# Performance work log

Hardware: AMD Instinct MI355X
Metric: run time of the kernel (lower is better)

## Reference

```python
import jax, jax.numpy as jnp
import numpy as np

NUM_HEADS = 16
WINDOW = 256  # local_window_size: query i attends keys in [i-WINDOW+1, i]


def setup_inputs() -> dict:
    key = jax.random.key(0)
    ks = jax.random.split(key, 7)
    B, L, D = 2, 2048, 1024
    s = 0.02  # typical init scale for projection weights
    return {
        "hidden_states": jax.random.normal(ks[0], (B, L, D), jnp.float32),
        "Wq": jax.random.normal(ks[1], (D, D), jnp.float32) * s,
        "bq": jnp.zeros((D,), jnp.float32),
        "Wk": jax.random.normal(ks[2], (D, D), jnp.float32) * s,
        "bk": jnp.zeros((D,), jnp.float32),
        "Wv": jax.random.normal(ks[3], (D, D), jnp.float32) * s,
        "bv": jnp.zeros((D,), jnp.float32),
    }


def reference(hidden_states, Wq, bq, Wk, bk, Wv, bv):
    B, L, D = hidden_states.shape
    H = NUM_HEADS
    dh = D // H

    def split_heads(x):  # [B,L,D] -> [B,H,L,dh]
        return x.reshape(B, L, H, dh).transpose(0, 2, 1, 3)

    q = split_heads(hidden_states @ Wq + bq)
    k = split_heads(hidden_states @ Wk + bk)
    v = split_heads(hidden_states @ Wv + bv)

    scores = jnp.einsum("bhqd,bhkd->bhqk", q, k) / jnp.sqrt(jnp.float32(dh))

    # causal sliding-window band: key j visible to query i iff i-WINDOW < j <= i
    i = jnp.arange(L)[:, None]
    j = jnp.arange(L)[None, :]
    band = (j <= i) & (j > i - WINDOW)
    scores = jnp.where(band, scores, -jnp.inf)

    probs = jax.nn.softmax(scores, axis=-1)  # dropout p=0 (eval)
    out = jnp.einsum("bhqk,bhkd->bhqd", probs, v)
    return out.transpose(0, 2, 1, 3).reshape(B, L, D)
```

## Files before the change

### kernel.cpp

```cpp
#include <hip/hip_runtime.h>
#include <hip/hip_bf16.h>
#include <stdint.h>
#include <math.h>

typedef __bf16 bf16;
typedef bf16  bf16x4  __attribute__((ext_vector_type(4)));
typedef bf16  bf16x8  __attribute__((ext_vector_type(8)));
typedef float floatx4 __attribute__((ext_vector_type(4)));

#define MFMA_16x16x32_BF16(a, b, c) \
  __builtin_amdgcn_mfma_f32_16x16x32_bf16((a), (b), (c), 0, 0, 0)

__device__ __forceinline__ int imin(int a, int b) { return a < b ? a : b; }
__device__ __forceinline__ int imax(int a, int b) { return a > b ? a : b; }

__device__ __forceinline__ void load_lds16(const void* g, void* l) {
  __builtin_amdgcn_global_load_lds(
      (const __attribute__((address_space(1))) unsigned int*)g,
      (__attribute__((address_space(3))) unsigned int*)l, 16, 0, 0);
}

#define LSEQ 2048
#define DMODEL 1024
#define NH 16
#define DH 64

__global__ void pack_all(const float4* __restrict__ x, uint16_t* __restrict__ y,
                         const float* __restrict__ Wq, const float* __restrict__ Wk,
                         const float* __restrict__ Wv, uint16_t* __restrict__ Wt) {
  const int bi = blockIdx.x;
  if (bi < 4096) {
    int i = bi * 256 + threadIdx.x;
    float4 f = x[i];
    bf16x4 v;
    v[0] = (bf16)f.x; v[1] = (bf16)f.y; v[2] = (bf16)f.z; v[3] = (bf16)f.w;
    *(bf16x4*)&y[(size_t)i * 4] = v;
    return;
  }
  __shared__ float tile[32][33];
  const int p = bi - 4096;
  const int z = p >> 10;
  const int rem = p & 1023;
  const int k0 = (rem >> 5) * 32, n0 = (rem & 31) * 32;
  const float* W = (z == 0) ? Wq : (z == 1) ? Wk : Wv;
  const int tx = threadIdx.x & 31, ty = threadIdx.x >> 5;
#pragma unroll
  for (int i = 0; i < 4; ++i)
    tile[ty + i * 8][tx] = W[(size_t)(k0 + ty + i * 8) * DMODEL + n0 + tx];
  __syncthreads();
  uint16_t* out = Wt + (size_t)z * DMODEL * DMODEL;
#pragma unroll
  for (int i = 0; i < 4; ++i)
    *(bf16*)&out[(size_t)(n0 + ty + i * 8) * DMODEL + k0 + tx] =
        (bf16)tile[tx][ty + i * 8];
}

__global__ __launch_bounds__(256, 3) void qkv_gemm(
    const uint16_t* __restrict__ A, const uint16_t* __restrict__ Wt,
    const float* __restrict__ bq, const float* __restrict__ bk,
    const float* __restrict__ bv,
    uint16_t* __restrict__ outq, uint16_t* __restrict__ outk,
    uint16_t* __restrict__ outvt) {
  __shared__ __attribute__((aligned(16))) uint16_t lds[17408];
  const int xcd = blockIdx.x & 7;
  const int i = blockIdx.x >> 3;
  const int m0 = (xcd * 4 + (i & 3)) * 128;
  const int rest = i >> 2;
  const int n0 = (rest & 7) * 128;
  const int z = rest >> 3;
  const uint16_t* Bt = Wt + (size_t)z * DMODEL * DMODEL;
  const float* bias = (z == 0) ? bq : (z == 1) ? bk : bv;

  const int t = threadIdx.x;
  const int lane = t & 63;
  const int wave = t >> 6;
  const int wm = (wave >> 1) * 64;
  const int wn = (wave & 1) * 64;
  const int col = lane & 15;
  const int quad = lane >> 4;

  floatx4 acc[4][4] = {};

  auto stage = [&](int kk, int bi) {
    const int k0 = kk * 32;
    uint16_t* base = &lds[bi * 8192];
#pragma unroll
    for (int c = 0; c < 4; ++c) {
      int chunk = t + c * 256;
      int cc = chunk & 511;
      int row = cc >> 2;
      int col16 = (cc & 3) ^ (row & 3);
      const uint16_t* g = (chunk < 512)
          ? A  + (size_t)(m0 + row) * DMODEL + k0 + col16 * 8
          : Bt + (size_t)(n0 + row) * DMODEL + k0 + col16 * 8;
      load_lds16(g, &base[chunk * 8]);
    }
  };

  stage(0, 0);
  for (int kk = 0; kk < 32; ++kk) {
    __syncthreads();
    if (kk < 31) stage(kk + 1, (kk + 1) & 1);
    const uint16_t* base = &lds[(kk & 1) * 8192];

    bf16x8 afrag[4], bfrag[4];
#pragma unroll
    for (int mi = 0; mi < 4; ++mi) {
      int r = wm + mi * 16 + col;
      afrag[mi] = *(const bf16x8*)&base[r * 32 + ((quad ^ (r & 3)) * 8)];
    }
#pragma unroll
    for (int nj = 0; nj < 4; ++nj) {
      int r = wn + nj * 16 + col;
      bfrag[nj] = *(const bf16x8*)&base[4096 + r * 32 + ((quad ^ (r & 3)) * 8)];
    }
#pragma unroll
    for (int mi = 0; mi < 4; ++mi)
#pragma unroll
      for (int nj = 0; nj < 4; ++nj)
        acc[mi][nj] = MFMA_16x16x32_BF16(afrag[mi], bfrag[nj], acc[mi][nj]);
  }

  if (z != 2) {
    const float scale = (z == 0) ? 0.125f : 1.0f;
    uint16_t* outp = (z == 0) ? outq : outk;
#pragma unroll
    for (int nj = 0; nj < 4; ++nj) {
      int gn = n0 + wn + nj * 16 + col;
      float bb = bias[gn];
      int h = gn >> 6, d = gn & 63;
#pragma unroll
      for (int mi = 0; mi < 4; ++mi) {
#pragma unroll
        for (int r = 0; r < 4; ++r) {
          int gm = m0 + wm + mi * 16 + quad * 4 + r;
          int b = gm >> 11, l = gm & 2047;
          *(bf16*)&outp[(((size_t)b * NH + h) * LSEQ + l) * DH + d] =
              (bf16)((acc[mi][nj][r] + bb) * scale);
        }
      }
    }
  } else {
    __syncthreads();
#pragma unroll
    for (int nj = 0; nj < 4; ++nj) {
      int n = wn + nj * 16 + col;
      float bb = bias[n0 + n];
#pragma unroll
      for (int mi = 0; mi < 4; ++mi) {
        int mb = wm + mi * 16 + quad * 4;
        int pp = (mb & ~31) | (((mb >> 2) & 3) << 3) | (((mb >> 4) & 1) << 2);
#pragma unroll
        for (int r = 0; r < 4; ++r)
          *(bf16*)&lds[n * 136 + pp + r] = (bf16)(acc[mi][nj][r] + bb);
      }
    }
    __syncthreads();
    const int n = t >> 1, mh = (t & 1) * 64;
    const int gn = n0 + n, d = gn & 63, h = gn >> 6;
    const int b = m0 >> 11, l0 = (m0 & 2047) + mh;
    uint16_t* dst = &outvt[(((size_t)b * NH + h) * DH + d) * LSEQ + l0];
    const uint16_t* src = &lds[n * 136 + mh];
#pragma unroll
    for (int j = 0; j < 8; ++j)
      *(bf16x8*)&dst[j * 8] = *(const bf16x8*)&src[j * 8];
  }
}

__global__ __launch_bounds__(256, 4) void attn(
    const uint16_t* __restrict__ Q, const uint16_t* __restrict__ K,
    const uint16_t* __restrict__ Vt, float* __restrict__ out) {
  __shared__ __attribute__((aligned(16))) uint16_t kbuf[2][4096];
  __shared__ __attribute__((aligned(16))) uint16_t vbuf[2][4096];

  const int t = threadIdx.x;
  const int lane = t & 63;
  const int w = t >> 6;
  const int xcd = blockIdx.x & 7;
  const int slot = blockIdx.x >> 3;
  const int bh = xcd * 4 + (slot >> 5);
  const int q0 = (slot & 31) * 64;
  const int q0w = q0 + w * 16;
  const int b = bh >> 4, h = bh & 15;
  const uint16_t* Qp = Q + (size_t)bh * LSEQ * DH;
  const uint16_t* Kp = K + (size_t)bh * LSEQ * DH;
  const uint16_t* Vp = Vt + (size_t)bh * DH * LSEQ;
  const int col = lane & 15, quad = lane >> 4;

  bf16x8 qf0 = *(const bf16x8*)&Qp[(size_t)(q0w + col) * DH + quad * 8];
  bf16x8 qf1 = *(const bf16x8*)&Qp[(size_t)(q0w + col) * DH + 32 + quad * 8];

  bf16x8 ones;
#pragma unroll
  for (int u = 0; u < 8; ++u) ones[u] = (bf16)1.0f;

  const int c_start = (q0 < 256) ? ((256 - q0) >> 6) : 0;

  floatx4 o[4] = {};
  floatx4 lac = {0.f, 0.f, 0.f, 0.f};

  auto stage = [&](int c, int bi) {
    const int kc = q0 - 256 + 64 * c;
    int ci = w * 64 + lane;
    {
      int row = ci >> 3, s = ci & 7;
      const uint16_t* g = Kp + (size_t)(kc + row) * DH + ((s ^ (row & 7)) * 8);
      load_lds16(g, &kbuf[bi][w * 512]);
      int row2 = row + 32;
      const uint16_t* g2 = Kp + (size_t)(kc + row2) * DH + ((s ^ (row2 & 7)) * 8);
      load_lds16(g2, &kbuf[bi][2048 + w * 512]);
    }
    {
      int d = ci >> 3, s = ci & 7;
      const uint16_t* g = Vp + (size_t)d * LSEQ + kc + ((s ^ (d & 7)) * 8);
      load_lds16(g, &vbuf[bi][w * 512]);
      int d2 = d + 32;
      const uint16_t* g2 = Vp + (size_t)d2 * LSEQ + kc + ((s ^ (d2 & 7)) * 8);
      load_lds16(g2, &vbuf[bi][2048 + w * 512]);
    }
  };

  stage(c_start, c_start & 1);

  for (int c = c_start; c <= 4; ++c) {
    __syncthreads();
    if (c < 4) stage(c + 1, (c + 1) & 1);

    const int kc = q0 - 256 + 64 * c;
    const int hi = q0w + 15, lo = q0w - 255;
    if (kc <= hi && kc + 64 > lo) {
      const uint16_t* kb_ = kbuf[c & 1];
      const uint16_t* vb_ = vbuf[c & 1];

      floatx4 sT[4] = {{0,0,0,0},{0,0,0,0},{0,0,0,0},{0,0,0,0}};
#pragma unroll
      for (int sub = 0; sub < 4; ++sub) {
        int r_ = sub * 16 + col;
        bf16x8 ka  = *(const bf16x8*)&kb_[r_ * 64 + ((quad ^ (r_ & 7)) * 8)];
        bf16x8 kb2 = *(const bf16x8*)&kb_[r_ * 64 + (((4 + quad) ^ (r_ & 7)) * 8)];
        sT[sub] = MFMA_16x16x32_BF16(ka, qf0, sT[sub]);
        sT[sub] = MFMA_16x16x32_BF16(kb2, qf1, sT[sub]);
      }

      const bool needm = (kc < q0w - 240) | (kc + 63 > q0w);
      const int q = q0w + col;
      bf16x8 pb[2];
#pragma unroll
      for (int sel = 0; sel < 2; ++sel) {
#pragma unroll
        for (int sp = 0; sp < 2; ++sp) {
#pragma unroll
          for (int r = 0; r < 4; ++r) {
            float v = sT[sel * 2 + sp][r];
            if (needm) {
              int key = kc + sel * 32 + sp * 16 + quad * 4 + r;
              v = ((key <= q) & (key > q - 256)) ? v : -INFINITY;
            }
            pb[sel][sp * 4 + r] = (bf16)__expf(v);
          }
        }
      }

#pragma unroll
      for (int nj = 0; nj < 4; ++nj) {
        int d = nj * 16 + col;
        bf16x8 va0 = *(const bf16x8*)&vb_[d * 64 + ((quad ^ (d & 7)) * 8)];
        bf16x8 va1 = *(const bf16x8*)&vb_[d * 64 + (((4 + quad) ^ (d & 7)) * 8)];
        o[nj] = MFMA_16x16x32_BF16(va0, pb[0], o[nj]);
        o[nj] = MFMA_16x16x32_BF16(va1, pb[1], o[nj]);
      }
      lac = MFMA_16x16x32_BF16(ones, pb[0], lac);
      lac = MFMA_16x16x32_BF16(ones, pb[1], lac);
    }
  }

  float rinv = 1.0f / lac[0];
#pragma unroll
  for (int nj = 0; nj < 4; ++nj) {
    float4 v4;
    v4.x = o[nj][0] * rinv; v4.y = o[nj][1] * rinv;
    v4.z = o[nj][2] * rinv; v4.w = o[nj][3] * rinv;
    *(float4*)&out[((size_t)b * LSEQ + q0w + col) * DMODEL + h * DH + nj * 16 + quad * 4] = v4;
  }
}

extern "C" void kernel_launch(void* const* d_in, const int* in_sizes, int n_in,
                              void* d_out, int out_size, void* d_ws, size_t ws_size,
                              hipStream_t stream) {
  const float* hidden = (const float*)d_in[0];
  const float* Wq = (const float*)d_in[1];
  const float* bq = (const float*)d_in[2];
  const float* Wk = (const float*)d_in[3];
  const float* bk = (const float*)d_in[4];
  const float* Wv = (const float*)d_in[5];
  const float* bv = (const float*)d_in[6];
  float* out = (float*)d_out;

  char* ws = (char*)d_ws;
  uint16_t* hb  = (uint16_t*)(ws);
  uint16_t* Wt  = (uint16_t*)(ws + ((size_t)8  << 20));
  uint16_t* qb  = (uint16_t*)(ws + ((size_t)14 << 20));
  uint16_t* kb  = (uint16_t*)(ws + ((size_t)22 << 20));
  uint16_t* vtb = (uint16_t*)(ws + ((size_t)30 << 20));

  pack_all<<<7168, 256, 0, stream>>>((const float4*)hidden, hb, Wq, Wk, Wv, Wt);
  qkv_gemm<<<768, 256, 0, stream>>>(hb, Wt, bq, bk, bv, qb, kb, vtb);
  attn<<<1024, 256, 0, stream>>>(qb, kb, vtb, out);
}
```

Before: 133.7 us.

## Fuse fp32-to-bf16 conversion of activations into QKV GEMM; add MFMA setprio

The separate pass that converts the hidden states to bf16 is removed. The QKV GEMM now streams fp32 activation tiles into LDS with a new XOR swizzle and converts them to bf16 when building the MFMA fragments. This drops one kernel's full write and re-read of the activation tensor, but each GEMM block loads twice the A bytes and uses more LDS, which may lower occupancy. The attention kernel also raises wave priority around its MFMA sections so matrix work is scheduled ahead of the softmax exp code.

```diff
diff --git a/kernel.cpp b/kernel.cpp
--- a/kernel.cpp
+++ b/kernel.cpp
@@ -25,20 +25,10 @@
 #define NH 16
 #define DH 64
 
-__global__ void pack_all(const float4* __restrict__ x, uint16_t* __restrict__ y,
-                         const float* __restrict__ Wq, const float* __restrict__ Wk,
-                         const float* __restrict__ Wv, uint16_t* __restrict__ Wt) {
-  const int bi = blockIdx.x;
-  if (bi < 4096) {
-    int i = bi * 256 + threadIdx.x;
-    float4 f = x[i];
-    bf16x4 v;
-    v[0] = (bf16)f.x; v[1] = (bf16)f.y; v[2] = (bf16)f.z; v[3] = (bf16)f.w;
-    *(bf16x4*)&y[(size_t)i * 4] = v;
-    return;
-  }
+__global__ void pack_w(const float* __restrict__ Wq, const float* __restrict__ Wk,
+                       const float* __restrict__ Wv, uint16_t* __restrict__ Wt) {
   __shared__ float tile[32][33];
-  const int p = bi - 4096;
+  const int p = blockIdx.x;
   const int z = p >> 10;
   const int rem = p & 1023;
   const int k0 = (rem >> 5) * 32, n0 = (rem & 31) * 32;
@@ -56,12 +46,13 @@
 }
 
 __global__ __launch_bounds__(256, 3) void qkv_gemm(
-    const uint16_t* __restrict__ A, const uint16_t* __restrict__ Wt,
+    const float* __restrict__ A,
+    const uint16_t* __restrict__ Wt,
     const float* __restrict__ bq, const float* __restrict__ bk,
     const float* __restrict__ bv,
     uint16_t* __restrict__ outq, uint16_t* __restrict__ outk,
     uint16_t* __restrict__ outvt) {
-  __shared__ __attribute__((aligned(16))) uint16_t lds[17408];
+  __shared__ __attribute__((aligned(16))) uint16_t lds[24576];
   const int xcd = blockIdx.x & 7;
   const int i = blockIdx.x >> 3;
   const int m0 = (xcd * 4 + (i & 3)) * 128;
@@ -83,17 +74,22 @@
 
   auto stage = [&](int kk, int bi) {
     const int k0 = kk * 32;
-    uint16_t* base = &lds[bi * 8192];
-#pragma unroll
-    for (int c = 0; c < 4; ++c) {
+    uint16_t* base = &lds[bi * 12288];
+#pragma unroll
+    for (int c = 0; c < 6; ++c) {
       int chunk = t + c * 256;
-      int cc = chunk & 511;
-      int row = cc >> 2;
-      int col16 = (cc & 3) ^ (row & 3);
-      const uint16_t* g = (chunk < 512)
-          ? A  + (size_t)(m0 + row) * DMODEL + k0 + col16 * 8
-          : Bt + (size_t)(n0 + row) * DMODEL + k0 + col16 * 8;
-      load_lds16(g, &base[chunk * 8]);
+      if (chunk < 1024) {
+        int row = chunk >> 3, sl = chunk & 7;
+        int cg = sl ^ (row & 7);
+        const float* g = A + (size_t)(m0 + row) * DMODEL + k0 + cg * 4;
+        load_lds16(g, &base[chunk * 8]);
+      } else {
+        int cb = chunk - 1024;
+        int row = cb >> 2, sl = cb & 3;
+        int cg = sl ^ (row & 3) ^ ((row >> 2) & 1);
+        const uint16_t* g = Bt + (size_t)(n0 + row) * DMODEL + k0 + cg * 8;
+        load_lds16(g, &base[8192 + cb * 8]);
+      }
     }
   };
 
@@ -101,18 +97,27 @@
   for (int kk = 0; kk < 32; ++kk) {
     __syncthreads();
     if (kk < 31) stage(kk + 1, (kk + 1) & 1);
-    const uint16_t* base = &lds[(kk & 1) * 8192];
+    const uint16_t* base = &lds[(kk & 1) * 12288];
 
     bf16x8 afrag[4], bfrag[4];
 #pragma unroll
     for (int mi = 0; mi < 4; ++mi) {
       int r = wm + mi * 16 + col;
-      afrag[mi] = *(const bf16x8*)&base[r * 32 + ((quad ^ (r & 3)) * 8)];
+      int f = r & 7;
+      floatx4 fa = *(const floatx4*)&base[r * 64 + (((2 * quad) ^ f) * 8)];
+      floatx4 fb = *(const floatx4*)&base[r * 64 + (((2 * quad + 1) ^ f) * 8)];
+      bf16x8 af;
+      af[0] = (bf16)fa[0]; af[1] = (bf16)fa[1];
+      af[2] = (bf16)fa[2]; af[3] = (bf16)fa[3];
+      af[4] = (bf16)fb[0]; af[5] = (bf16)fb[1];
+      af[6] = (bf16)fb[2]; af[7] = (bf16)fb[3];
+      afrag[mi] = af;
     }
 #pragma unroll
     for (int nj = 0; nj < 4; ++nj) {
       int r = wn + nj * 16 + col;
-      bfrag[nj] = *(const bf16x8*)&base[4096 + r * 32 + ((quad ^ (r & 3)) * 8)];
+      int f = (r & 3) ^ ((r >> 2) & 1);
+      bfrag[nj] = *(const bf16x8*)&base[8192 + r * 32 + ((quad ^ f) * 8)];
     }
 #pragma unroll
     for (int mi = 0; mi < 4; ++mi)
@@ -233,6 +238,7 @@
       const uint16_t* vb_ = vbuf[c & 1];
 
       floatx4 sT[4] = {{0,0,0,0},{0,0,0,0},{0,0,0,0},{0,0,0,0}};
+      __builtin_amdgcn_s_setprio(1);
 #pragma unroll
       for (int sub = 0; sub < 4; ++sub) {
         int r_ = sub * 16 + col;
@@ -241,6 +247,7 @@
         sT[sub] = MFMA_16x16x32_BF16(ka, qf0, sT[sub]);
         sT[sub] = MFMA_16x16x32_BF16(kb2, qf1, sT[sub]);
       }
+      __builtin_amdgcn_s_setprio(0);
 
       const bool needm = (kc < q0w - 240) | (kc + 63 > q0w);
       const int q = q0w + col;
@@ -261,6 +268,7 @@
         }
       }
 
+      __builtin_amdgcn_s_setprio(1);
 #pragma unroll
       for (int nj = 0; nj < 4; ++nj) {
         int d = nj * 16 + col;
@@ -271,6 +279,7 @@
       }
       lac = MFMA_16x16x32_BF16(ones, pb[0], lac);
       lac = MFMA_16x16x32_BF16(ones, pb[1], lac);
+      __builtin_amdgcn_s_setprio(0);
     }
   }
 
@@ -297,13 +306,12 @@
   float* out = (float*)d_out;
 
   char* ws = (char*)d_ws;
-  uint16_t* hb  = (uint16_t*)(ws);
-  uint16_t* Wt  = (uint16_t*)(ws + ((size_t)8  << 20));
-  uint16_t* qb  = (uint16_t*)(ws + ((size_t)14 << 20));
-  uint16_t* kb  = (uint16_t*)(ws + ((size_t)22 << 20));
-  uint16_t* vtb = (uint16_t*)(ws + ((size_t)30 << 20));
-
-  pack_all<<<7168, 256, 0, stream>>>((const float4*)hidden, hb, Wq, Wk, Wv, Wt);
-  qkv_gemm<<<768, 256, 0, stream>>>(hb, Wt, bq, bk, bv, qb, kb, vtb);
+  uint16_t* Wt  = (uint16_t*)(ws);
+  uint16_t* qb  = (uint16_t*)(ws + ((size_t)6  << 20));
+  uint16_t* kb  = (uint16_t*)(ws + ((size_t)14 << 20));
+  uint16_t* vtb = (uint16_t*)(ws + ((size_t)22 << 20));
+
+  pack_w<<<3072, 256, 0, stream>>>(Wq, Wk, Wv, Wt);
+  qkv_gemm<<<768, 256, 0, stream>>>(hidden, Wt, bq, bk, bv, qb, kb, vtb);
   attn<<<1024, 256, 0, stream>>>(qb, kb, vtb, out);
 }
```

After: 136.4 us. 1.02x slower.

## Rewrite QKV GEMM with 256x256 tiles, 8 waves, and phased ping-pong schedule

Applied to the files above, without the earlier changes.

Replaces the 128x128-tile QKV GEMM (768 blocks of 256 threads) with 256x256 tiles using 512 threads and a K-step of 64. Loads of the next A and B tiles are split across phases of the compute, with explicit waitcnt, barriers and raised wave priority around MFMA bursts. The aim is more operand reuse per LDS read and better overlap of global loads with MFMA. Only 192 blocks are launched, which may underfill the CUs. The attention kernel also gets setprio hints around its MFMA sections.

```diff
diff --git a/kernel.cpp b/kernel.cpp
--- a/kernel.cpp
+++ b/kernel.cpp
@@ -10,9 +10,6 @@
 
 #define MFMA_16x16x32_BF16(a, b, c) \
   __builtin_amdgcn_mfma_f32_16x16x32_bf16((a), (b), (c), 0, 0, 0)
-
-__device__ __forceinline__ int imin(int a, int b) { return a < b ? a : b; }
-__device__ __forceinline__ int imax(int a, int b) { return a > b ? a : b; }
 
 __device__ __forceinline__ void load_lds16(const void* g, void* l) {
   __builtin_amdgcn_global_load_lds(
@@ -55,71 +52,152 @@
         (bf16)tile[tx][ty + i * 8];
 }
 
-__global__ __launch_bounds__(256, 3) void qkv_gemm(
+__global__ __launch_bounds__(512, 2) void qkv_gemm8(
     const uint16_t* __restrict__ A, const uint16_t* __restrict__ Wt,
     const float* __restrict__ bq, const float* __restrict__ bk,
     const float* __restrict__ bv,
     uint16_t* __restrict__ outq, uint16_t* __restrict__ outk,
     uint16_t* __restrict__ outvt) {
-  __shared__ __attribute__((aligned(16))) uint16_t lds[17408];
+  __shared__ __attribute__((aligned(16))) uint16_t lds[65536];
+
   const int xcd = blockIdx.x & 7;
   const int i = blockIdx.x >> 3;
-  const int m0 = (xcd * 4 + (i & 3)) * 128;
-  const int rest = i >> 2;
-  const int n0 = (rest & 7) * 128;
-  const int z = rest >> 3;
+  const int m0 = (xcd * 2 + (i & 1)) * 256;
+  const int nz = i >> 1;
+  const int n0 = (nz & 3) * 256;
+  const int z = nz >> 2;
   const uint16_t* Bt = Wt + (size_t)z * DMODEL * DMODEL;
   const float* bias = (z == 0) ? bq : (z == 1) ? bk : bv;
 
   const int t = threadIdx.x;
   const int lane = t & 63;
-  const int wave = t >> 6;
-  const int wm = (wave >> 1) * 64;
-  const int wn = (wave & 1) * 64;
+  const int w = t >> 6;
+  const int wm = (w >> 2) * 128;
+  const int wn = (w & 3) * 64;
   const int col = lane & 15;
   const int quad = lane >> 4;
 
-  floatx4 acc[4][4] = {};
-
-  auto stage = [&](int kk, int bi) {
-    const int k0 = kk * 32;
-    uint16_t* base = &lds[bi * 8192];
+  floatx4 acc[8][4] = {};
+
+  auto stage = [&](int kt, int bi, int part) {
+    const int k0 = kt * 64;
+    uint16_t* base = &lds[bi * 32768 + part * 16384];
+    const uint16_t* src = part ? (Bt + (size_t)n0 * DMODEL)
+                               : (A  + (size_t)m0 * DMODEL);
 #pragma unroll
     for (int c = 0; c < 4; ++c) {
-      int chunk = t + c * 256;
-      int cc = chunk & 511;
-      int row = cc >> 2;
-      int col16 = (cc & 3) ^ (row & 3);
-      const uint16_t* g = (chunk < 512)
-          ? A  + (size_t)(m0 + row) * DMODEL + k0 + col16 * 8
-          : Bt + (size_t)(n0 + row) * DMODEL + k0 + col16 * 8;
+      int chunk = t + c * 512;
+      int row = chunk >> 3, sl = chunk & 7;
+      const uint16_t* g = src + (size_t)row * DMODEL + k0 + ((sl ^ (row & 7)) * 8);
       load_lds16(g, &base[chunk * 8]);
     }
   };
 
-  stage(0, 0);
-  for (int kk = 0; kk < 32; ++kk) {
-    __syncthreads();
-    if (kk < 31) stage(kk + 1, (kk + 1) & 1);
-    const uint16_t* base = &lds[(kk & 1) * 8192];
-
-    bf16x8 afrag[4], bfrag[4];
-#pragma unroll
-    for (int mi = 0; mi < 4; ++mi) {
+  stage(0, 0, 0);
+  stage(0, 0, 1);
+  asm volatile("s_waitcnt vmcnt(0)" ::: "memory");
+  __builtin_amdgcn_s_barrier();
+
+  bf16x8 af[8];
+  for (int kt = 0; kt < 16; ++kt) {
+    const uint16_t* buf = &lds[(kt & 1) * 32768];
+    const int nbi = (kt + 1) & 1;
+
+    if (kt < 15) {
+      stage(kt + 1, nbi, 0);
+      asm volatile("s_waitcnt vmcnt(4)" ::: "memory");
+    } else {
+      asm volatile("s_waitcnt vmcnt(0)" ::: "memory");
+    }
+    __builtin_amdgcn_s_barrier();
+    __builtin_amdgcn_sched_barrier(0);
+#pragma unroll
+    for (int mi = 0; mi < 8; ++mi) {
       int r = wm + mi * 16 + col;
-      afrag[mi] = *(const bf16x8*)&base[r * 32 + ((quad ^ (r & 3)) * 8)];
-    }
-#pragma unroll
-    for (int nj = 0; nj < 4; ++nj) {
-      int r = wn + nj * 16 + col;
-      bfrag[nj] = *(const bf16x8*)&base[4096 + r * 32 + ((quad ^ (r & 3)) * 8)];
-    }
-#pragma unroll
-    for (int mi = 0; mi < 4; ++mi)
-#pragma unroll
-      for (int nj = 0; nj < 4; ++nj)
-        acc[mi][nj] = MFMA_16x16x32_BF16(afrag[mi], bfrag[nj], acc[mi][nj]);
-  }
+      af[mi] = *(const bf16x8*)&buf[r * 64 + ((quad ^ (r & 7)) * 8)];
+    }
+    {
+      bf16x8 b0, b1;
+      {
+        int r = wn + col;
+        b0 = *(const bf16x8*)&buf[16384 + r * 64 + ((quad ^ (r & 7)) * 8)];
+        int r1 = wn + 16 + col;
+        b1 = *(const bf16x8*)&buf[16384 + r1 * 64 + ((quad ^ (r1 & 7)) * 8)];
+      }
+      __builtin_amdgcn_s_setprio(1);
+#pragma unroll
+      for (int mi = 0; mi < 8; ++mi) {
+        acc[mi][0] = MFMA_16x16x32_BF16(af[mi], b0, acc[mi][0]);
+        acc[mi][1] = MFMA_16x16x32_BF16(af[mi], b1, acc[mi][1]);
+      }
+      __builtin_amdgcn_s_setprio(0);
+    }
+    __builtin_amdgcn_s_barrier();
+
+    if (kt < 15) stage(kt + 1, nbi, 1);
+    __builtin_amdgcn_s_barrier();
+    {
+      bf16x8 b2, b3;
+      {
+        int r = wn + 32 + col;
+        b2 = *(const bf16x8*)&buf[16384 + r * 64 + ((quad ^ (r & 7)) * 8)];
+        int r1 = wn + 48 + col;
+        b3 = *(const bf16x8*)&buf[16384 + r1 * 64 + ((quad ^ (r1 & 7)) * 8)];
+      }
+      __builtin_amdgcn_s_setprio(1);
+#pragma unroll
+      for (int mi = 0; mi < 8; ++mi) {
+        acc[mi][2] = MFMA_16x16x32_BF16(af[mi], b2, acc[mi][2]);
+        acc[mi][3] = MFMA_16x16x32_BF16(af[mi], b3, acc[mi][3]);
+      }
+      __builtin_amdgcn_s_setprio(0);
+    }
+    __builtin_amdgcn_s_barrier();
+
+    __builtin_amdgcn_s_barrier();
+#pragma unroll
+    for (int mi = 0; mi < 8; ++mi) {
+      int r = wm + mi * 16 + col;
+      af[mi] = *(const bf16x8*)&buf[r * 64 + (((4 + quad) ^ (r & 7)) * 8)];
+    }
+    {
+      bf16x8 b0, b1;
+      {
+        int r = wn + col;
+        b0 = *(const bf16x8*)&buf[16384 + r * 64 + (((4 + quad) ^ (r & 7)) * 8)];
+        int r1 = wn + 16 + col;
+        b1 = *(const bf16x8*)&buf[16384 + r1 * 64 + (((4 + quad) ^ (r1 & 7)) * 8)];
+      }
+      __builtin_amdgcn_s_setprio(1);
+#pragma unroll
+      for (int mi = 0; mi < 8; ++mi) {
+        acc[mi][0] = MFMA_16x16x32_BF16(af[mi], b0, acc[mi][0]);
+        acc[mi][1] = MFMA_16x16x32_BF16(af[mi], b1, acc[mi][1]);
+      }
+      __builtin_amdgcn_s_setprio(0);
+    }
+    __builtin_amdgcn_s_barrier();
+
+    __builtin_amdgcn_s_barrier();
+    {
+      bf16x8 b2, b3;
+      {
+        int r = wn + 32 + col;
+        b2 = *(const bf16x8*)&buf[16384 + r * 64 + (((4 + quad) ^ (r & 7)) * 8)];
+        int r1 = wn + 48 + col;
+        b3 = *(const bf16x8*)&buf[16384 + r1 * 64 + (((4 + quad) ^ (r1 & 7)) * 8)];
+      }
+      __builtin_amdgcn_s_setprio(1);
+#pragma unroll
+      for (int mi = 0; mi < 8; ++mi) {
+        acc[mi][2] = MFMA_16x16x32_BF16(af[mi], b2, acc[mi][2]);
+        acc[mi][3] = MFMA_16x16x32_BF16(af[mi], b3, acc[mi][3]);
+      }
+      __builtin_amdgcn_s_setprio(0);
+    }
+    __builtin_amdgcn_s_barrier();
+  }
+  __builtin_amdgcn_s_barrier();
 
   if (z != 2) {
     const float scale = (z == 0) ? 0.125f : 1.0f;
@@ -130,7 +208,7 @@
       float bb = bias[gn];
       int h = gn >> 6, d = gn & 63;
 #pragma unroll
-      for (int mi = 0; mi < 4; ++mi) {
+      for (int mi = 0; mi < 8; ++mi) {
 #pragma unroll
         for (int r = 0; r < 4; ++r) {
           int gm = m0 + wm + mi * 16 + quad * 4 + r;
@@ -141,29 +219,37 @@
       }
     }
   } else {
-    __syncthreads();
-#pragma unroll
-    for (int nj = 0; nj < 4; ++nj) {
-      int n = wn + nj * 16 + col;
-      float bb = bias[n0 + n];
-#pragma unroll
-      for (int mi = 0; mi < 4; ++mi) {
-        int mb = wm + mi * 16 + quad * 4;
-        int pp = (mb & ~31) | (((mb >> 2) & 3) << 3) | (((mb >> 4) & 1) << 2);
-#pragma unroll
-        for (int r = 0; r < 4; ++r)
-          *(bf16*)&lds[n * 136 + pp + r] = (bf16)(acc[mi][nj][r] + bb);
-      }
-    }
-    __syncthreads();
-    const int n = t >> 1, mh = (t & 1) * 64;
-    const int gn = n0 + n, d = gn & 63, h = gn >> 6;
-    const int b = m0 >> 11, l0 = (m0 & 2047) + mh;
-    uint16_t* dst = &outvt[(((size_t)b * NH + h) * DH + d) * LSEQ + l0];
-    const uint16_t* src = &lds[n * 136 + mh];
-#pragma unroll
-    for (int j = 0; j < 8; ++j)
-      *(bf16x8*)&dst[j * 8] = *(const bf16x8*)&src[j * 8];
+    const int b = m0 >> 11;
+#pragma unroll
+    for (int H = 0; H < 2; ++H) {
+      if (wm == H * 128) {
+#pragma unroll
+        for (int nj = 0; nj < 4; ++nj) {
+          int n = wn + nj * 16 + col;
+          float bb = bias[n0 + n];
+#pragma unroll
+          for (int mi = 0; mi < 8; ++mi) {
+            int mb = mi * 16 + quad * 4;
+            int pp = (mb & ~31) | (((mb >> 2) & 3) << 3) | (((mb >> 4) & 1) << 2);
+#pragma unroll
+            for (int r = 0; r < 4; ++r)
+              *(bf16*)&lds[n * 136 + pp + r] = (bf16)(acc[mi][nj][r] + bb);
+          }
+        }
+      }
+      __syncthreads();
+      {
+        const int n = t >> 1, mh = (t & 1) * 64;
+        const int gn = n0 + n, d = gn & 63, h = gn >> 6;
+        const int l0 = (m0 & 2047) + H * 128 + mh;
+        uint16_t* dst = &outvt[(((size_t)b * NH + h) * DH + d) * LSEQ + l0];
+        const uint16_t* src = &lds[n * 136 + mh];
+#pragma unroll
+        for (int j = 0; j < 8; ++j)
+          *(bf16x8*)&dst[j * 8] = *(const bf16x8*)&src[j * 8];
+      }
+      __syncthreads();
+    }
   }
 }
 
@@ -233,6 +319,7 @@
       const uint16_t* vb_ = vbuf[c & 1];
 
       floatx4 sT[4] = {{0,0,0,0},{0,0,0,0},{0,0,0,0},{0,0,0,0}};
+      __builtin_amdgcn_s_setprio(1);
 #pragma unroll
       for (int sub = 0; sub < 4; ++sub) {
         int r_ = sub * 16 + col;
@@ -241,6 +328,7 @@
         sT[sub] = MFMA_16x16x32_BF16(ka, qf0, sT[sub]);
         sT[sub] = MFMA_16x16x32_BF16(kb2, qf1, sT[sub]);
       }
+      __builtin_amdgcn_s_setprio(0);
 
       const bool needm = (kc < q0w - 240) | (kc + 63 > q0w);
       const int q = q0w + col;
@@ -261,6 +349,7 @@
         }
       }
 
+      __builtin_amdgcn_s_setprio(1);
 #pragma unroll
       for (int nj = 0; nj < 4; ++nj) {
         int d = nj * 16 + col;
@@ -271,6 +360,7 @@
       }
       lac = MFMA_16x16x32_BF16(ones, pb[0], lac);
       lac = MFMA_16x16x32_BF16(ones, pb[1], lac);
+      __builtin_amdgcn_s_setprio(0);
     }
   }
 
@@ -304,6 +394,6 @@
   uint16_t* vtb = (uint16_t*)(ws + ((size_t)30 << 20));
 
   pack_all<<<7168, 256, 0, stream>>>((const float4*)hidden, hb, Wq, Wk, Wv, Wt);
-  qkv_gemm<<<768, 256, 0, stream>>>(hb, Wt, bq, bk, bv, qb, kb, vtb);
+  qkv_gemm8<<<192, 512, 0, stream>>>(hb, Wt, bq, bk, bv, qb, kb, vtb);
   attn<<<1024, 256, 0, stream>>>(qb, kb, vtb, out);
 }
```

Measured after the change: 139.2 us. 4.1% more time.

## Retile QKV GEMM to 128x192 with K=64 stages, split V transpose out

Applied to the files above, without the earlier changes.

The QKV GEMM now uses 128x192 output tiles spanning the concatenated Q/K/V weight columns, with 64-wide K stages and a 512-block grid. Pipelining is done with explicit waitcnt, barriers and raised wave priority around the MFMA blocks. The V transpose moves out of the GEMM epilogue into a separate vtrans kernel, which adds a launch and an extra round trip of V through memory. MFMA sections in the attention kernel also get setprio hints. The larger tile uses more LDS and registers, which lowers occupancy to two blocks per CU.

```diff
diff --git a/kernel.cpp b/kernel.cpp
--- a/kernel.cpp
+++ b/kernel.cpp
@@ -10,9 +10,6 @@
 
 #define MFMA_16x16x32_BF16(a, b, c) \
   __builtin_amdgcn_mfma_f32_16x16x32_bf16((a), (b), (c), 0, 0, 0)
-
-__device__ __forceinline__ int imin(int a, int b) { return a < b ? a : b; }
-__device__ __forceinline__ int imax(int a, int b) { return a > b ? a : b; }
 
 __device__ __forceinline__ void load_lds16(const void* g, void* l) {
   __builtin_amdgcn_global_load_lds(
@@ -55,116 +52,144 @@
         (bf16)tile[tx][ty + i * 8];
 }
 
-__global__ __launch_bounds__(256, 3) void qkv_gemm(
+__global__ __launch_bounds__(256, 2) void qkv_gemm(
     const uint16_t* __restrict__ A, const uint16_t* __restrict__ Wt,
     const float* __restrict__ bq, const float* __restrict__ bk,
     const float* __restrict__ bv,
     uint16_t* __restrict__ outq, uint16_t* __restrict__ outk,
-    uint16_t* __restrict__ outvt) {
-  __shared__ __attribute__((aligned(16))) uint16_t lds[17408];
+    uint16_t* __restrict__ outv) {
+  __shared__ __attribute__((aligned(16))) uint16_t lds[40960];
+
   const int xcd = blockIdx.x & 7;
   const int i = blockIdx.x >> 3;
   const int m0 = (xcd * 4 + (i & 3)) * 128;
-  const int rest = i >> 2;
-  const int n0 = (rest & 7) * 128;
-  const int z = rest >> 3;
-  const uint16_t* Bt = Wt + (size_t)z * DMODEL * DMODEL;
-  const float* bias = (z == 0) ? bq : (z == 1) ? bk : bv;
+  const int n0 = (i >> 2) * 192;
 
   const int t = threadIdx.x;
   const int lane = t & 63;
-  const int wave = t >> 6;
-  const int wm = (wave >> 1) * 64;
-  const int wn = (wave & 1) * 64;
+  const int w = t >> 6;
+  const int wm = (w >> 1) * 64;
+  const int wn = (w & 1) * 96;
   const int col = lane & 15;
   const int quad = lane >> 4;
 
-  floatx4 acc[4][4] = {};
-
-  auto stage = [&](int kk, int bi) {
-    const int k0 = kk * 32;
-    uint16_t* base = &lds[bi * 8192];
-#pragma unroll
-    for (int c = 0; c < 4; ++c) {
+  floatx4 acc[4][6] = {};
+
+  auto stage = [&](int kt, int bi) {
+    const int k0 = kt * 64;
+    uint16_t* base = &lds[bi * 20480];
+#pragma unroll
+    for (int c = 0; c < 10; ++c) {
       int chunk = t + c * 256;
-      int cc = chunk & 511;
-      int row = cc >> 2;
-      int col16 = (cc & 3) ^ (row & 3);
-      const uint16_t* g = (chunk < 512)
-          ? A  + (size_t)(m0 + row) * DMODEL + k0 + col16 * 8
-          : Bt + (size_t)(n0 + row) * DMODEL + k0 + col16 * 8;
-      load_lds16(g, &base[chunk * 8]);
+      if (chunk < 1024) {
+        int row = chunk >> 3, sl = chunk & 7;
+        const uint16_t* g =
+            A + (size_t)(m0 + row) * DMODEL + k0 + ((sl ^ (row & 7)) * 8);
+        load_lds16(g, &base[chunk * 8]);
+      } else {
+        int cb = chunk - 1024;
+        int row = cb >> 3, sl = cb & 7;
+        int gc = n0 + row;
+        const uint16_t* g = Wt + ((size_t)(gc >> 10) << 20) +
+                            (size_t)(gc & 1023) * DMODEL + k0 +
+                            ((sl ^ (row & 7)) * 8);
+        load_lds16(g, &base[8192 + cb * 8]);
+      }
     }
   };
 
   stage(0, 0);
-  for (int kk = 0; kk < 32; ++kk) {
-    __syncthreads();
-    if (kk < 31) stage(kk + 1, (kk + 1) & 1);
-    const uint16_t* base = &lds[(kk & 1) * 8192];
-
-    bf16x8 afrag[4], bfrag[4];
+  for (int kt = 0; kt < 16; ++kt) {
+    const uint16_t* buf = &lds[(kt & 1) * 20480];
+
+    asm volatile("s_waitcnt vmcnt(0)" ::: "memory");
+    __builtin_amdgcn_s_barrier();
+    __builtin_amdgcn_sched_barrier(0);
+    if (kt < 15) stage(kt + 1, (kt + 1) & 1);
+    __builtin_amdgcn_sched_barrier(0);
+
+    bf16x8 a0[4], b0[6], a1[4], b1[6];
 #pragma unroll
     for (int mi = 0; mi < 4; ++mi) {
       int r = wm + mi * 16 + col;
-      afrag[mi] = *(const bf16x8*)&base[r * 32 + ((quad ^ (r & 3)) * 8)];
-    }
-#pragma unroll
-    for (int nj = 0; nj < 4; ++nj) {
+      a0[mi] = *(const bf16x8*)&buf[r * 64 + ((quad ^ (r & 7)) * 8)];
+    }
+#pragma unroll
+    for (int nj = 0; nj < 6; ++nj) {
       int r = wn + nj * 16 + col;
-      bfrag[nj] = *(const bf16x8*)&base[4096 + r * 32 + ((quad ^ (r & 3)) * 8)];
-    }
+      b0[nj] = *(const bf16x8*)&buf[8192 + r * 64 + ((quad ^ (r & 7)) * 8)];
+    }
+#pragma unroll
+    for (int mi = 0; mi < 4; ++mi) {
+      int r = wm + mi * 16 + col;
+      a1[mi] = *(const bf16x8*)&buf[r * 64 + (((4 + quad) ^ (r & 7)) * 8)];
+    }
+#pragma unroll
+    for (int nj = 0; nj < 6; ++nj) {
+      int r = wn + nj * 16 + col;
+      b1[nj] = *(const bf16x8*)&buf[8192 + r * 64 + (((4 + quad) ^ (r & 7)) * 8)];
+    }
+
+    __builtin_amdgcn_s_setprio(1);
 #pragma unroll
     for (int mi = 0; mi < 4; ++mi)
 #pragma unroll
-      for (int nj = 0; nj < 4; ++nj)
-        acc[mi][nj] = MFMA_16x16x32_BF16(afrag[mi], bfrag[nj], acc[mi][nj]);
-  }
-
-  if (z != 2) {
-    const float scale = (z == 0) ? 0.125f : 1.0f;
-    uint16_t* outp = (z == 0) ? outq : outk;
-#pragma unroll
-    for (int nj = 0; nj < 4; ++nj) {
-      int gn = n0 + wn + nj * 16 + col;
-      float bb = bias[gn];
-      int h = gn >> 6, d = gn & 63;
-#pragma unroll
-      for (int mi = 0; mi < 4; ++mi) {
-#pragma unroll
-        for (int r = 0; r < 4; ++r) {
-          int gm = m0 + wm + mi * 16 + quad * 4 + r;
-          int b = gm >> 11, l = gm & 2047;
-          *(bf16*)&outp[(((size_t)b * NH + h) * LSEQ + l) * DH + d] =
-              (bf16)((acc[mi][nj][r] + bb) * scale);
-        }
-      }
-    }
-  } else {
-    __syncthreads();
-#pragma unroll
-    for (int nj = 0; nj < 4; ++nj) {
-      int n = wn + nj * 16 + col;
-      float bb = bias[n0 + n];
-#pragma unroll
-      for (int mi = 0; mi < 4; ++mi) {
-        int mb = wm + mi * 16 + quad * 4;
-        int pp = (mb & ~31) | (((mb >> 2) & 3) << 3) | (((mb >> 4) & 1) << 2);
-#pragma unroll
-        for (int r = 0; r < 4; ++r)
-          *(bf16*)&lds[n * 136 + pp + r] = (bf16)(acc[mi][nj][r] + bb);
-      }
-    }
-    __syncthreads();
-    const int n = t >> 1, mh = (t & 1) * 64;
-    const int gn = n0 + n, d = gn & 63, h = gn >> 6;
-    const int b = m0 >> 11, l0 = (m0 & 2047) + mh;
-    uint16_t* dst = &outvt[(((size_t)b * NH + h) * DH + d) * LSEQ + l0];
-    const uint16_t* src = &lds[n * 136 + mh];
-#pragma unroll
-    for (int j = 0; j < 8; ++j)
-      *(bf16x8*)&dst[j * 8] = *(const bf16x8*)&src[j * 8];
-  }
+      for (int nj = 0; nj < 6; ++nj)
+        acc[mi][nj] = MFMA_16x16x32_BF16(a0[mi], b0[nj], acc[mi][nj]);
+    __builtin_amdgcn_s_setprio(0);
+    __builtin_amdgcn_s_setprio(1);
+#pragma unroll
+    for (int mi = 0; mi < 4; ++mi)
+#pragma unroll
+      for (int nj = 0; nj < 6; ++nj)
+        acc[mi][nj] = MFMA_16x16x32_BF16(a1[mi], b1[nj], acc[mi][nj]);
+    __builtin_amdgcn_s_setprio(0);
+  }
+
+#pragma unroll
+  for (int nj = 0; nj < 6; ++nj) {
+    int gc = n0 + wn + nj * 16 + col;
+    int zz = gc >> 10, rem = gc & 1023;
+    const float* biasp = (zz == 0) ? bq : (zz == 1) ? bk : bv;
+    uint16_t* outp = (zz == 0) ? outq : (zz == 1) ? outk : outv;
+    const float scale = (zz == 0) ? 0.125f : 1.0f;
+    float bb = biasp[rem];
+    int h = rem >> 6, d = rem & 63;
+#pragma unroll
+    for (int mi = 0; mi < 4; ++mi) {
+#pragma unroll
+      for (int r = 0; r < 4; ++r) {
+        int gm = m0 + wm + mi * 16 + quad * 4 + r;
+        int b = gm >> 11, l = gm & 2047;
+        *(bf16*)&outp[(((size_t)b * NH + h) * LSEQ + l) * DH + d] =
+            (bf16)((acc[mi][nj][r] + bb) * scale);
+      }
+    }
+  }
+}
+
+__global__ __launch_bounds__(256) void vtrans(const uint16_t* __restrict__ V,
+                                              uint16_t* __restrict__ Vt) {
+  __shared__ uint16_t tl[64 * 68];
+  const int t = threadIdx.x;
+  const int bh = blockIdx.x >> 5;
+  const int l0 = (blockIdx.x & 31) * 64;
+  const uint16_t* src = V + ((size_t)bh * LSEQ + l0) * DH;
+
+  const int l = t >> 2, dc = (t & 3) * 16;
+  bf16x8 v0 = *(const bf16x8*)&src[(size_t)l * DH + dc];
+  bf16x8 v1 = *(const bf16x8*)&src[(size_t)l * DH + dc + 8];
+  const int pp = (l & 32) | (((l >> 2) & 3) << 3) | (((l >> 4) & 1) << 2) | (l & 3);
+#pragma unroll
+  for (int j = 0; j < 8; ++j) {
+    tl[(dc + j) * 68 + pp]     = ((const uint16_t*)&v0)[j];
+    tl[(dc + 8 + j) * 68 + pp] = ((const uint16_t*)&v1)[j];
+  }
+  __syncthreads();
+  const int d = t >> 2, lc = (t & 3) * 16;
+  uint16_t* dst = Vt + ((size_t)bh * DH + d) * LSEQ + l0 + lc;
+  *(bf16x8*)&dst[0] = *(const bf16x8*)&tl[d * 68 + lc];
+  *(bf16x8*)&dst[8] = *(const bf16x8*)&tl[d * 68 + lc + 8];
 }
 
 __global__ __launch_bounds__(256, 4) void attn(
@@ -233,6 +258,7 @@
       const uint16_t* vb_ = vbuf[c & 1];
 
       floatx4 sT[4] = {{0,0,0,0},{0,0,0,0},{0,0,0,0},{0,0,0,0}};
+      __builtin_amdgcn_s_setprio(1);
 #pragma unroll
       for (int sub = 0; sub < 4; ++sub) {
         int r_ = sub * 16 + col;
@@ -241,6 +267,7 @@
         sT[sub] = MFMA_16x16x32_BF16(ka, qf0, sT[sub]);
         sT[sub] = MFMA_16x16x32_BF16(kb2, qf1, sT[sub]);
       }
+      __builtin_amdgcn_s_setprio(0);
 
       const bool needm = (kc < q0w - 240) | (kc + 63 > q0w);
       const int q = q0w + col;
@@ -261,6 +288,7 @@
         }
       }
 
+      __builtin_amdgcn_s_setprio(1);
 #pragma unroll
       for (int nj = 0; nj < 4; ++nj) {
         int d = nj * 16 + col;
@@ -271,6 +299,7 @@
       }
       lac = MFMA_16x16x32_BF16(ones, pb[0], lac);
       lac = MFMA_16x16x32_BF16(ones, pb[1], lac);
+      __builtin_amdgcn_s_setprio(0);
     }
   }
 
@@ -301,9 +330,11 @@
   uint16_t* Wt  = (uint16_t*)(ws + ((size_t)8  << 20));
   uint16_t* qb  = (uint16_t*)(ws + ((size_t)14 << 20));
   uint16_t* kb  = (uint16_t*)(ws + ((size_t)22 << 20));
-  uint16_t* vtb = (uint16_t*)(ws + ((size_t)30 << 20));
+  uint16_t* vb  = (uint16_t*)(ws + ((size_t)30 << 20));
+  uint16_t* vtb = (uint16_t*)(ws + ((size_t)38 << 20));
 
   pack_all<<<7168, 256, 0, stream>>>((const float4*)hidden, hb, Wq, Wk, Wv, Wt);
-  qkv_gemm<<<768, 256, 0, stream>>>(hb, Wt, bq, bk, bv, qb, kb, vtb);
+  qkv_gemm<<<512, 256, 0, stream>>>(hb, Wt, bq, bk, bv, qb, kb, vb);
+  vtrans<<<1024, 256, 0, stream>>>(vb, vtb);
   attn<<<1024, 256, 0, stream>>>(qb, kb, vtb, out);
 }
```

New measurement: 127.2 us, median of 2. -4.8%, faster.
